# Kernel optimization log

Measured on AMD Instinct MI355X. Metric: run time of the kernel, lower is better.

The kernel has to match this reference:

```python
import jax, jax.numpy as jnp
import numpy as np
from math import sqrt

B, T, I, H, O, R = 128, 1000, 3, 512, 1, 2
NOISE_STD = 0.05
ALPHA = 0.2


def setup_inputs() -> dict:
    key = jax.random.key(0)
    ks = jax.random.split(key, 6)
    inp = jax.random.normal(ks[0], (B, T, I), dtype=jnp.float32)
    noise = jax.random.normal(ks[1], (B, T, H), dtype=jnp.float32)
    # parameters initialized as in the torch module
    wi = jax.random.normal(ks[2], (I, H), dtype=jnp.float32)
    si = jnp.ones((I,), dtype=jnp.float32)
    m = jax.random.normal(ks[3], (H, R), dtype=jnp.float32) * (1.0 / sqrt(H))
    n = jax.random.normal(ks[4], (H, R), dtype=jnp.float32) * (1.0 / sqrt(H))
    wo = jax.random.normal(ks[5], (H, O), dtype=jnp.float32) * (2.0 / H)
    so = jnp.ones((O,), dtype=jnp.float32)
    h0 = jnp.zeros((H,), dtype=jnp.float32)
    return {"input": inp, "noise": noise, "wi": wi, "si": si, "m": m,
            "n": n, "wo": wo, "so": so, "h0": h0}


def reference(input, noise, wi, si, m, n, wo, so, h0):
    # proxy parameters: wi_full = (wi.T * si).T, wo_full = wo * so
    wi_full = si[:, None] * wi          # (I, H)
    wo_full = wo * so                   # (H, O)
    batch = input.shape[0]
    h_init = jnp.broadcast_to(h0, (batch, h0.shape[0]))  # (B, H)

    def step(h, xs):
        x_t, z_t = xs                   # (B, I), (B, H)
        r = jnp.tanh(h)
        rec = (r @ n) @ m.T             # low-rank recurrence, (B, H)
        h_new = h + NOISE_STD * z_t + ALPHA * (-h + rec + x_t @ wi_full)
        out = jnp.tanh(h_new) @ wo_full  # (B, O)
        return h_new, (out, h_new)

    xs = (jnp.swapaxes(input, 0, 1), jnp.swapaxes(noise, 0, 1))  # time-major
    _, (outs, hs) = jax.lax.scan(step, h_init, xs)
    output = jnp.swapaxes(outs, 0, 1)               # (B, T, O)
    trajectories = jnp.concatenate(
        [h_init[:, None, :], jnp.swapaxes(hs, 0, 1)], axis=1)  # (B, T+1, H)
    return output, trajectories
```

## Files before the change

kernel.cpp:

```cpp
#include <hip/hip_runtime.h>
#include <stdint.h>

#define B_ 128
#define T_ 1000
#define H_ 512
#define PH 8
#define NPHASE 125

typedef float vfloat4 __attribute__((ext_vector_type(4)));

template <int CTRL>
__device__ __forceinline__ float dpp_add(float x) {
    int moved = __builtin_amdgcn_update_dpp(0, __float_as_int(x), CTRL, 0xf, 0xf, true);
    return x + __int_as_float(moved);
}

__device__ __forceinline__ void wave_reduce2(float& p0, float& p1) {
    p0 = dpp_add<0x111>(p0); p1 = dpp_add<0x111>(p1);
    p0 = dpp_add<0x112>(p0); p1 = dpp_add<0x112>(p1);
    p0 = dpp_add<0x114>(p0); p1 = dpp_add<0x114>(p1);
    p0 = dpp_add<0x118>(p0); p1 = dpp_add<0x118>(p1);
    p0 = dpp_add<0x142>(p0); p1 = dpp_add<0x142>(p1);
    p0 = dpp_add<0x143>(p0); p1 = dpp_add<0x143>(p1);
}

__device__ __forceinline__ float wave_reduce1(float p) {
    p = dpp_add<0x111>(p); p = dpp_add<0x112>(p); p = dpp_add<0x114>(p);
    p = dpp_add<0x118>(p); p = dpp_add<0x142>(p); p = dpp_add<0x143>(p);
    return p;
}

__device__ __forceinline__ float fast_tanh(float x) {
    float E = __builtin_amdgcn_exp2f(x * 2.885390081777927f);
    float r = __builtin_amdgcn_rcpf(E + 1.0f);
    return __builtin_fmaf(-2.0f, r, 1.0f);
}

__global__ __launch_bounds__(128, 1) void lowrank_rnn_kernel(
    const float* __restrict__ input,
    const float* __restrict__ noise,
    const float* __restrict__ wi,
    const float* __restrict__ si,
    const float* __restrict__ m,
    const float* __restrict__ n,
    const float* __restrict__ wo,
    const float* __restrict__ so,
    const float* __restrict__ h0,
    float* __restrict__ out)
{
    const int b    = blockIdx.x;
    const int tid  = threadIdx.x;
    const int wid  = tid >> 6;
    const int lane = tid & 63;
    const int j0   = lane * 8;

    __shared__ __align__(16) vfloat4 ub[2][PH][2][64];
    __shared__ __align__(16) vfloat4 rb[2][PH][2][64];
    __shared__ __align__(16) vfloat4 hb[2][PH][2][64];
    __shared__ __align__(16) vfloat4 rfin[2][64];
    __shared__ float os[T_ + 1];
    __shared__ int   flags[2];

    if (tid == 0) { flags[0] = 0; flags[1] = 0; }
    __syncthreads();
    volatile int* vprod = &flags[0];
    volatile int* vcons = &flags[1];

    if (wid == 1) {
        float wS0[8], wS1[8], wS2[8], wof[8];
        {
            const float so0 = so[0];
            #pragma unroll
            for (int i = 0; i < 3; ++i) {
                float s = 0.2f * si[i];
                float* dst = (i == 0) ? wS0 : (i == 1) ? wS1 : wS2;
                #pragma unroll
                for (int q = 0; q < 2; ++q) {
                    vfloat4 vw = *(const vfloat4*)(wi + i * H_ + j0 + 4 * q);
                    dst[4*q] = vw.x * s; dst[4*q+1] = vw.y * s;
                    dst[4*q+2] = vw.z * s; dst[4*q+3] = vw.w * s;
                }
            }
            #pragma unroll
            for (int q = 0; q < 2; ++q) {
                vfloat4 vw = *(const vfloat4*)(wo + j0 + 4 * q);
                wof[4*q] = vw.x * so0; wof[4*q+1] = vw.y * so0;
                wof[4*q+2] = vw.z * so0; wof[4*q+3] = vw.w * so0;
            }
        }
        const float* zb = noise + (size_t)b * T_ * H_ + j0;
        const float* xb = input + (size_t)b * T_ * 3;
        float* trajBase = out + (size_t)B_ * T_ + (size_t)b * (T_ + 1) * H_;

        {
            vfloat4 a = *(const vfloat4*)(h0 + j0);
            vfloat4 c = *(const vfloat4*)(h0 + j0 + 4);
            *(vfloat4*)(trajBase + j0)     = a;
            *(vfloat4*)(trajBase + j0 + 4) = c;
        }

        auto emit_phase = [&](int pp) {
            const int hf = pp & 1;
            #pragma unroll
            for (int s = 0; s < PH; ++s) {
                const int t = pp * PH + s;
                vfloat4 rl = rb[hf][s][0][lane];
                vfloat4 rh = rb[hf][s][1][lane];
                float p2 = rl.x * wof[0];
                p2 = __builtin_fmaf(rl.y, wof[1], p2);
                p2 = __builtin_fmaf(rl.z, wof[2], p2);
                p2 = __builtin_fmaf(rl.w, wof[3], p2);
                p2 = __builtin_fmaf(rh.x, wof[4], p2);
                p2 = __builtin_fmaf(rh.y, wof[5], p2);
                p2 = __builtin_fmaf(rh.z, wof[6], p2);
                p2 = __builtin_fmaf(rh.w, wof[7], p2);
                p2 = wave_reduce1(p2);
                if (lane == 63) os[t] = p2;
                vfloat4 hl = hb[hf][s][0][lane];
                vfloat4 hh = hb[hf][s][1][lane];
                float* tr = trajBase + (size_t)(t + 1) * H_ + j0;
                *(vfloat4*)tr       = hl;
                *(vfloat4*)(tr + 4) = hh;
            }
        };

        for (int q = 0; q < NPHASE; ++q) {
            if (q >= 2) {
                while (*vcons < q - 1) {}
                asm volatile("" ::: "memory");
            }
            vfloat4 zl[PH], zh[PH];
            #pragma unroll
            for (int s = 0; s < PH; ++s) {
                const float* g = zb + (size_t)(q * PH + s) * H_;
                zl[s] = *(const vfloat4*)g;
                zh[s] = *(const vfloat4*)(g + 4);
            }
            if (q >= 2) emit_phase(q - 2);
            const int half = q & 1;
            #pragma unroll
            for (int s = 0; s < PH; ++s) {
                const int t = q * PH + s;
                float x0 = xb[3*t], x1 = xb[3*t+1], x2 = xb[3*t+2];
                float zz[8] = {zl[s].x, zl[s].y, zl[s].z, zl[s].w,
                               zh[s].x, zh[s].y, zh[s].z, zh[s].w};
                float u[8];
                #pragma unroll
                for (int k = 0; k < 8; ++k) {
                    float xw = __builtin_fmaf(x0, wS0[k],
                               __builtin_fmaf(x1, wS1[k], x2 * wS2[k]));
                    u[k] = __builtin_fmaf(zz[k], 0.05f, xw);
                }
                vfloat4 ulo = {u[0], u[1], u[2], u[3]};
                vfloat4 uhi = {u[4], u[5], u[6], u[7]};
                ub[half][s][0][lane] = ulo;
                ub[half][s][1][lane] = uhi;
            }
            asm volatile("s_waitcnt lgkmcnt(0)" ::: "memory");
            if (lane == 0) *vprod = q + 1;
        }
        while (*vcons < NPHASE) {}
        asm volatile("" ::: "memory");
        emit_phase(NPHASE - 2);
        emit_phase(NPHASE - 1);
        while (*vcons < NPHASE + 1) {}
        asm volatile("" ::: "memory");
        {
            vfloat4 rl = rfin[0][lane], rh = rfin[1][lane];
            float p2 = rl.x * wof[0];
            p2 = __builtin_fmaf(rl.y, wof[1], p2);
            p2 = __builtin_fmaf(rl.z, wof[2], p2);
            p2 = __builtin_fmaf(rl.w, wof[3], p2);
            p2 = __builtin_fmaf(rh.x, wof[4], p2);
            p2 = __builtin_fmaf(rh.y, wof[5], p2);
            p2 = __builtin_fmaf(rh.z, wof[6], p2);
            p2 = __builtin_fmaf(rh.w, wof[7], p2);
            p2 = wave_reduce1(p2);
            if (lane == 63) os[T_] = p2;
        }
        asm volatile("s_waitcnt lgkmcnt(0)" ::: "memory");
        float* outp = out + (size_t)b * T_;
        for (int idx = lane; idx < T_; idx += 64)
            outp[idx] = os[idx + 1];
    } else {
        float h[8], n0[8], n1[8], m0S[8], m1S[8];
        {
            const float* nb = n + 2 * j0;
            const float* mb = m + 2 * j0;
            #pragma unroll
            for (int q = 0; q < 4; ++q) {
                vfloat4 vn = *(const vfloat4*)(nb + 4 * q);
                n0[2*q] = vn.x; n1[2*q] = vn.y; n0[2*q+1] = vn.z; n1[2*q+1] = vn.w;
                vfloat4 vm = *(const vfloat4*)(mb + 4 * q);
                m0S[2*q] = 0.2f * vm.x;   m1S[2*q] = 0.2f * vm.y;
                m0S[2*q+1] = 0.2f * vm.z; m1S[2*q+1] = 0.2f * vm.w;
            }
            #pragma unroll
            for (int q = 0; q < 2; ++q) {
                vfloat4 vh = *(const vfloat4*)(h0 + j0 + 4 * q);
                h[4*q] = vh.x; h[4*q+1] = vh.y; h[4*q+2] = vh.z; h[4*q+3] = vh.w;
            }
        }

        for (int p = 0; p < NPHASE; ++p) {
            while (*vprod < p + 1) {}
            asm volatile("" ::: "memory");
            const int half = p & 1;
            vfloat4 cul = ub[half][0][0][lane];
            vfloat4 cuh = ub[half][0][1][lane];
            #pragma unroll
            for (int s = 0; s < PH; ++s) {
                vfloat4 nul, nuh;
                if (s < PH - 1) {
                    nul = ub[half][s+1][0][lane];
                    nuh = ub[half][s+1][1][lane];
                }
                float r[8];
                #pragma unroll
                for (int k = 0; k < 8; ++k) r[k] = fast_tanh(h[k]);

                float p0 = r[0] * n0[0], p1 = r[0] * n1[0];
                #pragma unroll
                for (int k = 1; k < 8; ++k) {
                    p0 = __builtin_fmaf(r[k], n0[k], p0);
                    p1 = __builtin_fmaf(r[k], n1[k], p1);
                }
                wave_reduce2(p0, p1);

                float uu[8] = {cul.x, cul.y, cul.z, cul.w, cuh.x, cuh.y, cuh.z, cuh.w};
                float base[8];
                #pragma unroll
                for (int k = 0; k < 8; ++k)
                    base[k] = __builtin_fmaf(h[k], 0.8f, uu[k]);

                float a0 = __int_as_float(__builtin_amdgcn_readlane(__float_as_int(p0), 63));
                float a1 = __int_as_float(__builtin_amdgcn_readlane(__float_as_int(p1), 63));

                #pragma unroll
                for (int k = 0; k < 8; ++k)
                    h[k] = __builtin_fmaf(a0, m0S[k], __builtin_fmaf(a1, m1S[k], base[k]));

                vfloat4 rlo = {r[0], r[1], r[2], r[3]};
                vfloat4 rhi = {r[4], r[5], r[6], r[7]};
                rb[half][s][0][lane] = rlo;
                rb[half][s][1][lane] = rhi;
                vfloat4 hlo = {h[0], h[1], h[2], h[3]};
                vfloat4 hhi = {h[4], h[5], h[6], h[7]};
                hb[half][s][0][lane] = hlo;
                hb[half][s][1][lane] = hhi;

                cul = nul; cuh = nuh;
            }
            asm volatile("s_waitcnt lgkmcnt(0)" ::: "memory");
            if (lane == 0) *vcons = p + 1;
        }
        while (*vprod < NPHASE) {}
        asm volatile("" ::: "memory");
        float r[8];
        #pragma unroll
        for (int k = 0; k < 8; ++k) r[k] = fast_tanh(h[k]);
        vfloat4 rlo = {r[0], r[1], r[2], r[3]};
        vfloat4 rhi = {r[4], r[5], r[6], r[7]};
        rfin[0][lane] = rlo;
        rfin[1][lane] = rhi;
        asm volatile("s_waitcnt lgkmcnt(0)" ::: "memory");
        if (lane == 0) *vcons = NPHASE + 1;
    }
}

extern "C" void kernel_launch(void* const* d_in, const int* in_sizes, int n_in,
                              void* d_out, int out_size, void* d_ws, size_t ws_size,
                              hipStream_t stream) {
    const float* input = (const float*)d_in[0];
    const float* noise = (const float*)d_in[1];
    const float* wi    = (const float*)d_in[2];
    const float* si    = (const float*)d_in[3];
    const float* m     = (const float*)d_in[4];
    const float* n     = (const float*)d_in[5];
    const float* wo    = (const float*)d_in[6];
    const float* so    = (const float*)d_in[7];
    const float* h0    = (const float*)d_in[8];
    float* out = (float*)d_out;

    hipLaunchKernelGGL(lowrank_rnn_kernel, dim3(B_), dim3(128), 0, stream,
                       input, noise, wi, si, m, n, wo, so, h0, out);
}
```

Baseline: 295.8 us.

## Precompute tanh of base term off critical path and correct with polynomial

Splits h into base plus a low-rank correction and computes the exp/rcp for tanh(base) ahead of the wave reduction. tanh(h) at the next step is then recovered by a cheap Taylor expansion of exp on the small correction plus a Newton-style reciprocal refinement. The aim is to take the transcendental latency off the serial recurrence chain. The product sum is also rebalanced into a tree. This is an approximation whose accuracy depends on the correction staying small.

New measurement: 376.1 us. +27.1%, slower.

```diff
diff --git a/kernel.cpp b/kernel.cpp
--- a/kernel.cpp
+++ b/kernel.cpp
@@ -35,6 +35,9 @@
     float r = __builtin_amdgcn_rcpf(E + 1.0f);
     return __builtin_fmaf(-2.0f, r, 1.0f);
 }
+
+#define C2_ 2.885390081777927f
+#define C6_ 0.16666666666666666f
 
 __global__ __launch_bounds__(128, 1) void lowrank_rnn_kernel(
     const float* __restrict__ input,
@@ -183,14 +186,14 @@
         for (int idx = lane; idx < T_; idx += 64)
             outp[idx] = os[idx + 1];
     } else {
-        float h[8], n0[8], n1[8], m0S[8], m1S[8];
+        float h[8], n0v[8], n1v[8], m0S[8], m1S[8], R0[8], S0[8];
         {
             const float* nb = n + 2 * j0;
             const float* mb = m + 2 * j0;
             #pragma unroll
             for (int q = 0; q < 4; ++q) {
                 vfloat4 vn = *(const vfloat4*)(nb + 4 * q);
-                n0[2*q] = vn.x; n1[2*q] = vn.y; n0[2*q+1] = vn.z; n1[2*q+1] = vn.w;
+                n0v[2*q] = vn.x; n1v[2*q] = vn.y; n0v[2*q+1] = vn.z; n1v[2*q+1] = vn.w;
                 vfloat4 vm = *(const vfloat4*)(mb + 4 * q);
                 m0S[2*q] = 0.2f * vm.x;   m1S[2*q] = 0.2f * vm.y;
                 m0S[2*q+1] = 0.2f * vm.z; m1S[2*q+1] = 0.2f * vm.w;
@@ -200,7 +203,14 @@
                 vfloat4 vh = *(const vfloat4*)(h0 + j0 + 4 * q);
                 h[4*q] = vh.x; h[4*q+1] = vh.y; h[4*q+2] = vh.z; h[4*q+3] = vh.w;
             }
-        }
+            #pragma unroll
+            for (int k = 0; k < 8; ++k) {
+                float eb = __builtin_amdgcn_exp2f(h[k] * C2_);
+                float r0 = __builtin_amdgcn_rcpf(eb + 1.0f);
+                R0[k] = r0; S0[k] = 1.0f - r0;
+            }
+        }
+        float a0T = 0.0f, a1T = 0.0f;
 
         for (int p = 0; p < NPHASE; ++p) {
             while (*vprod < p + 1) {}
@@ -217,28 +227,46 @@
                 }
                 float r[8];
                 #pragma unroll
-                for (int k = 0; k < 8; ++k) r[k] = fast_tanh(h[k]);
-
-                float p0 = r[0] * n0[0], p1 = r[0] * n1[0];
-                #pragma unroll
-                for (int k = 1; k < 8; ++k) {
-                    p0 = __builtin_fmaf(r[k], n0[k], p0);
-                    p1 = __builtin_fmaf(r[k], n1[k], p1);
-                }
-                wave_reduce2(p0, p1);
+                for (int k = 0; k < 8; ++k) {
+                    float v  = __builtin_fmaf(a0T, m0S[k], a1T * m1S[k]);
+                    float t1 = __builtin_fmaf(v, C6_, 0.5f);
+                    float t2 = __builtin_fmaf(v, t1, 1.0f);
+                    float em = v * t2;
+                    float g  = S0[k] * em;
+                    float w1 = 1.0f - g;
+                    float w2 = __builtin_fmaf(-g, w1, 1.0f);
+                    float q  = __builtin_fmaf(-g, w2, 1.0f);
+                    float qq = q + q;
+                    r[k] = __builtin_fmaf(-R0[k], qq, 1.0f);
+                }
+                float u0[8], u1[8];
+                #pragma unroll
+                for (int k = 0; k < 8; ++k) { u0[k] = r[k] * n0v[k]; u1[k] = r[k] * n1v[k]; }
+                float p0 = ((u0[0]+u0[1]) + (u0[2]+u0[3])) + ((u0[4]+u0[5]) + (u0[6]+u0[7]));
+                float p1 = ((u1[0]+u1[1]) + (u1[2]+u1[3])) + ((u1[4]+u1[5]) + (u1[6]+u1[7]));
 
                 float uu[8] = {cul.x, cul.y, cul.z, cul.w, cuh.x, cuh.y, cuh.z, cuh.w};
-                float base[8];
+                float base[8], R0n[8], S0n[8];
                 #pragma unroll
                 for (int k = 0; k < 8; ++k)
                     base[k] = __builtin_fmaf(h[k], 0.8f, uu[k]);
-
+                #pragma unroll
+                for (int k = 0; k < 8; ++k) {
+                    float eb = __builtin_amdgcn_exp2f(base[k] * C2_);
+                    float r0 = __builtin_amdgcn_rcpf(eb + 1.0f);
+                    R0n[k] = r0; S0n[k] = 1.0f - r0;
+                }
+
+                wave_reduce2(p0, p1);
                 float a0 = __int_as_float(__builtin_amdgcn_readlane(__float_as_int(p0), 63));
                 float a1 = __int_as_float(__builtin_amdgcn_readlane(__float_as_int(p1), 63));
 
                 #pragma unroll
                 for (int k = 0; k < 8; ++k)
                     h[k] = __builtin_fmaf(a0, m0S[k], __builtin_fmaf(a1, m1S[k], base[k]));
+                a0T = a0 + a0; a1T = a1 + a1;
+                #pragma unroll
+                for (int k = 0; k < 8; ++k) { R0[k] = R0n[k]; S0[k] = S0n[k]; }
 
                 vfloat4 rlo = {r[0], r[1], r[2], r[3]};
                 vfloat4 rhi = {r[4], r[5], r[6], r[7]};
```

## Break serial recurrence dependency with Taylor-linearized lookahead of low-rank coefficients

Applied to the files above, without the earlier changes.

The compute wave no longer waits on a full tanh, dot and wave reduction before each step. It precomputes tanh of a predicted next state two steps ahead and keeps a first-order correction, using a Jacobian-like 2x2 matrix refreshed every four steps. That matrix gives the rank-2 coefficients from already-reduced quantities, taking the cross-lane reduction off the per-step critical path. State is also packed into float2 vectors to allow packed math, and the trajectory indexing is shifted with a separate final-state buffer. The linearization is an approximation of tanh, so it adds numerical error and many more VALU operations per step.

Result: slower. 357.1 us (+20.7%).

```diff
diff --git a/kernel.cpp b/kernel.cpp
--- a/kernel.cpp
+++ b/kernel.cpp
@@ -8,6 +8,7 @@
 #define NPHASE 125
 
 typedef float vfloat4 __attribute__((ext_vector_type(4)));
+typedef float vfloat2 __attribute__((ext_vector_type(2)));
 
 template <int CTRL>
 __device__ __forceinline__ float dpp_add(float x) {
@@ -24,6 +25,15 @@
     p0 = dpp_add<0x143>(p0); p1 = dpp_add<0x143>(p1);
 }
 
+__device__ __forceinline__ void wave_reduce4(float& a, float& b, float& c, float& d) {
+    a = dpp_add<0x111>(a); b = dpp_add<0x111>(b); c = dpp_add<0x111>(c); d = dpp_add<0x111>(d);
+    a = dpp_add<0x112>(a); b = dpp_add<0x112>(b); c = dpp_add<0x112>(c); d = dpp_add<0x112>(d);
+    a = dpp_add<0x114>(a); b = dpp_add<0x114>(b); c = dpp_add<0x114>(c); d = dpp_add<0x114>(d);
+    a = dpp_add<0x118>(a); b = dpp_add<0x118>(b); c = dpp_add<0x118>(c); d = dpp_add<0x118>(d);
+    a = dpp_add<0x142>(a); b = dpp_add<0x142>(b); c = dpp_add<0x142>(c); d = dpp_add<0x142>(d);
+    a = dpp_add<0x143>(a); b = dpp_add<0x143>(b); c = dpp_add<0x143>(c); d = dpp_add<0x143>(d);
+}
+
 __device__ __forceinline__ float wave_reduce1(float p) {
     p = dpp_add<0x111>(p); p = dpp_add<0x112>(p); p = dpp_add<0x114>(p);
     p = dpp_add<0x118>(p); p = dpp_add<0x142>(p); p = dpp_add<0x143>(p);
@@ -36,17 +46,24 @@
     return __builtin_fmaf(-2.0f, r, 1.0f);
 }
 
+#define C2_ 2.885390081777927f
+#define RL63(x) __int_as_float(__builtin_amdgcn_readlane(__float_as_int(x), 63))
+
+__device__ __forceinline__ vfloat2 bc2(float x) { vfloat2 v = {x, x}; return v; }
+__device__ __forceinline__ vfloat2 th2(vfloat2 b) {
+    vfloat2 x2 = b * C2_;
+    vfloat2 E  = {__builtin_amdgcn_exp2f(x2.x), __builtin_amdgcn_exp2f(x2.y)};
+    vfloat2 D  = E + 1.0f;
+    vfloat2 R  = {__builtin_amdgcn_rcpf(D.x), __builtin_amdgcn_rcpf(D.y)};
+    return bc2(-2.0f) * R + 1.0f;
+}
+
 __global__ __launch_bounds__(128, 1) void lowrank_rnn_kernel(
-    const float* __restrict__ input,
-    const float* __restrict__ noise,
-    const float* __restrict__ wi,
-    const float* __restrict__ si,
-    const float* __restrict__ m,
-    const float* __restrict__ n,
-    const float* __restrict__ wo,
-    const float* __restrict__ so,
-    const float* __restrict__ h0,
-    float* __restrict__ out)
+    const float* __restrict__ input, const float* __restrict__ noise,
+    const float* __restrict__ wi, const float* __restrict__ si,
+    const float* __restrict__ m, const float* __restrict__ n,
+    const float* __restrict__ wo, const float* __restrict__ so,
+    const float* __restrict__ h0, float* __restrict__ out)
 {
     const int b    = blockIdx.x;
     const int tid  = threadIdx.x;
@@ -58,6 +75,7 @@
     __shared__ __align__(16) vfloat4 rb[2][PH][2][64];
     __shared__ __align__(16) vfloat4 hb[2][PH][2][64];
     __shared__ __align__(16) vfloat4 rfin[2][64];
+    __shared__ __align__(16) vfloat4 hfin[2][64];
     __shared__ float os[T_ + 1];
     __shared__ int   flags[2];
 
@@ -118,7 +136,7 @@
                 if (lane == 63) os[t] = p2;
                 vfloat4 hl = hb[hf][s][0][lane];
                 vfloat4 hh = hb[hf][s][1][lane];
-                float* tr = trajBase + (size_t)(t + 1) * H_ + j0;
+                float* tr = trajBase + (size_t)t * H_ + j0;
                 *(vfloat4*)tr       = hl;
                 *(vfloat4*)(tr + 4) = hh;
             }
@@ -177,94 +195,228 @@
             p2 = __builtin_fmaf(rh.w, wof[7], p2);
             p2 = wave_reduce1(p2);
             if (lane == 63) os[T_] = p2;
+            float* tr = trajBase + (size_t)T_ * H_ + j0;
+            *(vfloat4*)tr       = hfin[0][lane];
+            *(vfloat4*)(tr + 4) = hfin[1][lane];
         }
         asm volatile("s_waitcnt lgkmcnt(0)" ::: "memory");
         float* outp = out + (size_t)b * T_;
         for (int idx = lane; idx < T_; idx += 64)
             outp[idx] = os[idx + 1];
     } else {
-        float h[8], n0[8], n1[8], m0S[8], m1S[8];
+        vfloat2 m0S[4], m1S[4], n0v[4], n1v[4];
+        vfloat2 basep[4], Tk0[4], Tk1[4], Dk0[4], Dk1[4], ucur[4];
+        float cA0=0, cA1=0, cB0=0, cB1=0, qa0=0, qa1=0, qa2=0, qa3=0;
+        float A00, A01, A10, A11;
+        float a1_0, a1_1, a2_0, a2_1, C0cur, C1cur;
+        vfloat2 h0v[4];
         {
             const float* nb = n + 2 * j0;
             const float* mb = m + 2 * j0;
             #pragma unroll
             for (int q = 0; q < 4; ++q) {
                 vfloat4 vn = *(const vfloat4*)(nb + 4 * q);
-                n0[2*q] = vn.x; n1[2*q] = vn.y; n0[2*q+1] = vn.z; n1[2*q+1] = vn.w;
+                vfloat2 a = {vn.x, vn.z}; n0v[q] = a;
+                vfloat2 c = {vn.y, vn.w}; n1v[q] = c;
                 vfloat4 vm = *(const vfloat4*)(mb + 4 * q);
-                m0S[2*q] = 0.2f * vm.x;   m1S[2*q] = 0.2f * vm.y;
-                m0S[2*q+1] = 0.2f * vm.z; m1S[2*q+1] = 0.2f * vm.w;
+                vfloat2 d = {0.2f * vm.x, 0.2f * vm.z}; m0S[q] = d;
+                vfloat2 e = {0.2f * vm.y, 0.2f * vm.w}; m1S[q] = e;
             }
             #pragma unroll
             for (int q = 0; q < 2; ++q) {
                 vfloat4 vh = *(const vfloat4*)(h0 + j0 + 4 * q);
-                h[4*q] = vh.x; h[4*q+1] = vh.y; h[4*q+2] = vh.z; h[4*q+3] = vh.w;
-            }
-        }
-
-        for (int p = 0; p < NPHASE; ++p) {
+                vfloat2 lo = {vh.x, vh.y}, hi = {vh.z, vh.w};
+                h0v[2*q] = lo; h0v[2*q+1] = hi;
+            }
+        }
+        #define HORIZ(dst, A_, B_) { \
+            vfloat2 q01_ = A_[1]*B_[1] + A_[0]*B_[0]; \
+            vfloat2 q23_ = A_[3]*B_[3] + A_[2]*B_[2]; \
+            vfloat2 qq_ = q01_ + q23_; dst = qq_.x + qq_.y; }
+        #define SHIP(ring, hf, sl, V_) { \
+            vfloat4 lo_ = {V_[0].x, V_[0].y, V_[1].x, V_[1].y}; \
+            vfloat4 hi_ = {V_[2].x, V_[2].y, V_[3].x, V_[3].y}; \
+            ring[hf][sl][0][lane] = lo_; ring[hf][sl][1][lane] = hi_; }
+        #define RDU(dst, hf, sl) { \
+            vfloat4 lo_ = ub[hf][sl][0][lane]; vfloat4 hi_ = ub[hf][sl][1][lane]; \
+            vfloat2 t0_ = {lo_.x, lo_.y}; dst[0] = t0_; \
+            vfloat2 t1_ = {lo_.z, lo_.w}; dst[1] = t1_; \
+            vfloat2 t2_ = {hi_.x, hi_.y}; dst[2] = t2_; \
+            vfloat2 t3_ = {hi_.z, hi_.w}; dst[3] = t3_; }
+
+        while (*vprod < 1) {}
+        asm volatile("" ::: "memory");
+        vfloat2 u0v[4], u1v[4], u2v[4];
+        RDU(u0v, 0, 0); RDU(u1v, 0, 1); RDU(u2v, 0, 2);
+        float a0_0, a0_1;
+        {
+            vfloat2 r0v[4], T0v[4], D0v[4], base0c[4];
+            #pragma unroll
+            for (int j = 0; j < 4; ++j) r0v[j] = th2(h0v[j]);
+            SHIP(rb, 0, 0, r0v); SHIP(hb, 0, 0, h0v);
+            float p0, p1; HORIZ(p0, r0v, n0v); HORIZ(p1, r0v, n1v);
+            wave_reduce2(p0, p1);
+            a0_0 = RL63(p0); a0_1 = RL63(p1);
+            #pragma unroll
+            for (int j = 0; j < 4; ++j) { base0c[j] = h0v[j] * 0.8f + u0v[j]; basep[j] = base0c[j]; }
+            #pragma unroll
+            for (int j = 0; j < 4; ++j) { T0v[j] = th2(base0c[j]); D0v[j] = 1.0f - T0v[j]*T0v[j]; }
+            float c10, c11; HORIZ(c10, T0v, n0v); HORIZ(c11, T0v, n1v);
+            vfloat2 e0[4], e1[4];
+            #pragma unroll
+            for (int j = 0; j < 4; ++j) { e0[j] = D0v[j]*m0S[j]; e1[j] = D0v[j]*m1S[j]; }
+            float q0, q1, q2, q3;
+            HORIZ(q0, e0, n0v); HORIZ(q1, e1, n0v); HORIZ(q2, e0, n1v); HORIZ(q3, e1, n1v);
+            wave_reduce2(c10, c11); wave_reduce4(q0, q1, q2, q3);
+            float C1_0 = RL63(c10), C1_1 = RL63(c11);
+            A00 = RL63(q0); A01 = RL63(q1); A10 = RL63(q2); A11 = RL63(q3);
+            #pragma unroll
+            for (int j = 0; j < 4; ++j) {
+                vfloat2 be = base0c[j] * 0.8f + u1v[j];
+                vfloat2 T = th2(be); Tk0[j] = T; Dk0[j] = 1.0f - T*T;
+            }
+            HORIZ(cA0, Tk0, n0v); HORIZ(cA1, Tk0, n1v);
+            wave_reduce2(cA0, cA1);
+            float w0 = a0_0, w1 = a0_1;
+            float at0 = C1_0 + A00*w0 + A01*w1;
+            float at1 = C1_1 + A10*w0 + A11*w1;
+            vfloat2 ab0 = bc2(a0_0), ab1 = bc2(a0_1);
+            vfloat2 h1v[4], r1v[4];
+            #pragma unroll
+            for (int j = 0; j < 4; ++j) {
+                vfloat2 dl = ab0*m0S[j] + ab1*m1S[j];
+                h1v[j] = basep[j] + dl;
+                vfloat2 t1 = T0v[j]*dl;
+                vfloat2 ee = dl - t1*dl;
+                r1v[j] = D0v[j]*ee + T0v[j];
+            }
+            SHIP(hb, 0, 1, h1v); SHIP(rb, 0, 1, r1v);
+            #pragma unroll
+            for (int j = 0; j < 4; ++j) basep[j] = h1v[j]*0.8f + u1v[j];
+            #pragma unroll
+            for (int j = 0; j < 4; ++j) {
+                vfloat2 be = basep[j]*0.8f + u2v[j];
+                vfloat2 T = th2(be); Tk1[j] = T; Dk1[j] = 1.0f - T*T;
+            }
+            HORIZ(cB0, Tk1, n0v); HORIZ(cB1, Tk1, n1v);
+            wave_reduce2(cB0, cB1);
+            C0cur = RL63(cA0); C1cur = RL63(cA1);
+            a2_0 = a0_0; a2_1 = a0_1; a1_0 = at0; a1_1 = at1;
+            #pragma unroll
+            for (int j = 0; j < 4; ++j) ucur[j] = u2v[j];
+        }
+
+        #define CSTEP(S_, HF_, UH_, US_, SPIN_, RLA_) { \
+            if (SPIN_) { while (*vprod < (SPIN_)) {} asm volatile("" ::: "memory"); } \
+            vfloat2 unv[4]; RDU(unv, (UH_), (US_)); \
+            float Cn0, Cn1; \
+            if (((S_) & 1) == 0) { Cn0 = RL63(cB0); Cn1 = RL63(cB1); } \
+            else                 { Cn0 = RL63(cA0); Cn1 = RL63(cA1); } \
+            if (((S_) % 4) == 2 && (RLA_)) { \
+                A00 = RL63(qa0); A01 = RL63(qa1); A10 = RL63(qa2); A11 = RL63(qa3); } \
+            float w0 = __builtin_fmaf(0.8f, a2_0, a1_0); \
+            float w1 = __builtin_fmaf(0.8f, a2_1, a1_1); \
+            float at0 = __builtin_fmaf(A00, w0, __builtin_fmaf(A01, w1, C0cur)); \
+            float at1 = __builtin_fmaf(A10, w0, __builtin_fmaf(A11, w1, C1cur)); \
+            vfloat2 ab0 = bc2(a1_0), ab1 = bc2(a1_1); \
+            vfloat2 wb0 = bc2(w0),  wb1 = bc2(w1); \
+            vfloat2 hv[4], rv[4], Tn[4], Dn[4]; \
+            _Pragma("unroll") \
+            for (int j = 0; j < 4; ++j) { \
+                vfloat2 dl = ab0*m0S[j] + ab1*m1S[j]; \
+                hv[j] = basep[j] + dl; \
+                vfloat2 ep = wb0*m0S[j] + wb1*m1S[j]; \
+                vfloat2 Tp = ((S_) & 1) ? Tk1[j] : Tk0[j]; \
+                vfloat2 Dp = ((S_) & 1) ? Dk1[j] : Dk0[j]; \
+                vfloat2 t1 = Tp*ep; \
+                vfloat2 ee = ep - t1*ep; \
+                rv[j] = Dp*ee + Tp; \
+            } \
+            SHIP(hb, (HF_), (S_), hv); SHIP(rb, (HF_), (S_), rv); \
+            _Pragma("unroll") \
+            for (int j = 0; j < 4; ++j) { \
+                basep[j] = hv[j]*0.8f + ucur[j]; \
+                vfloat2 be = basep[j]*0.8f + unv[j]; \
+                vfloat2 T = th2(be); \
+                Tn[j] = T; Dn[j] = 1.0f - T*T; \
+                if ((S_) & 1) { Tk1[j] = T; Dk1[j] = Dn[j]; } \
+                else          { Tk0[j] = T; Dk0[j] = Dn[j]; } \
+                ucur[j] = unv[j]; \
+            } \
+            float pc0, pc1; HORIZ(pc0, Tn, n0v); HORIZ(pc1, Tn, n1v); \
+            if (((S_) & 1) == 0) { cA0 = pc0; cA1 = pc1; wave_reduce2(cA0, cA1); } \
+            else                 { cB0 = pc0; cB1 = pc1; wave_reduce2(cB0, cB1); } \
+            if (((S_) % 4) == 0) { \
+                vfloat2 e0[4], e1[4]; \
+                _Pragma("unroll") \
+                for (int j = 0; j < 4; ++j) { e0[j] = Dn[j]*m0S[j]; e1[j] = Dn[j]*m1S[j]; } \
+                HORIZ(qa0, e0, n0v); HORIZ(qa1, e1, n0v); \
+                HORIZ(qa2, e0, n1v); HORIZ(qa3, e1, n1v); \
+                wave_reduce4(qa0, qa1, qa2, qa3); \
+            } \
+            a2_0 = a1_0; a2_1 = a1_1; a1_0 = at0; a1_1 = at1; \
+            C0cur = Cn0; C1cur = Cn1; }
+
+        CSTEP(2, 0, 0, 3, 0, 0)
+        CSTEP(3, 0, 0, 4, 0, 1)
+        CSTEP(4, 0, 0, 5, 0, 1)
+        CSTEP(5, 0, 0, 6, 0, 1)
+        CSTEP(6, 0, 0, 7, 0, 1)
+        CSTEP(7, 0, 1, 0, 2, 1)
+        asm volatile("s_waitcnt lgkmcnt(0)" ::: "memory");
+        if (lane == 0) *vcons = 1;
+
+        for (int p = 1; p < NPHASE - 1; ++p) {
             while (*vprod < p + 1) {}
             asm volatile("" ::: "memory");
             const int half = p & 1;
-            vfloat4 cul = ub[half][0][0][lane];
-            vfloat4 cuh = ub[half][0][1][lane];
-            #pragma unroll
-            for (int s = 0; s < PH; ++s) {
-                vfloat4 nul, nuh;
-                if (s < PH - 1) {
-                    nul = ub[half][s+1][0][lane];
-                    nuh = ub[half][s+1][1][lane];
-                }
-                float r[8];
-                #pragma unroll
-                for (int k = 0; k < 8; ++k) r[k] = fast_tanh(h[k]);
-
-                float p0 = r[0] * n0[0], p1 = r[0] * n1[0];
-                #pragma unroll
-                for (int k = 1; k < 8; ++k) {
-                    p0 = __builtin_fmaf(r[k], n0[k], p0);
-                    p1 = __builtin_fmaf(r[k], n1[k], p1);
-                }
-                wave_reduce2(p0, p1);
-
-                float uu[8] = {cul.x, cul.y, cul.z, cul.w, cuh.x, cuh.y, cuh.z, cuh.w};
-                float base[8];
-                #pragma unroll
-                for (int k = 0; k < 8; ++k)
-                    base[k] = __builtin_fmaf(h[k], 0.8f, uu[k]);
-
-                float a0 = __int_as_float(__builtin_amdgcn_readlane(__float_as_int(p0), 63));
-                float a1 = __int_as_float(__builtin_amdgcn_readlane(__float_as_int(p1), 63));
-
-                #pragma unroll
-                for (int k = 0; k < 8; ++k)
-                    h[k] = __builtin_fmaf(a0, m0S[k], __builtin_fmaf(a1, m1S[k], base[k]));
-
-                vfloat4 rlo = {r[0], r[1], r[2], r[3]};
-                vfloat4 rhi = {r[4], r[5], r[6], r[7]};
-                rb[half][s][0][lane] = rlo;
-                rb[half][s][1][lane] = rhi;
-                vfloat4 hlo = {h[0], h[1], h[2], h[3]};
-                vfloat4 hhi = {h[4], h[5], h[6], h[7]};
-                hb[half][s][0][lane] = hlo;
-                hb[half][s][1][lane] = hhi;
-
-                cul = nul; cuh = nuh;
-            }
+            CSTEP(0, half, half, 1, 0, 1)
+            CSTEP(1, half, half, 2, 0, 1)
+            CSTEP(2, half, half, 3, 0, 1)
+            CSTEP(3, half, half, 4, 0, 1)
+            CSTEP(4, half, half, 5, 0, 1)
+            CSTEP(5, half, half, 6, 0, 1)
+            CSTEP(6, half, half, 7, 0, 1)
+            CSTEP(7, half, half ^ 1, 0, p + 2, 1)
             asm volatile("s_waitcnt lgkmcnt(0)" ::: "memory");
             if (lane == 0) *vcons = p + 1;
         }
-        while (*vprod < NPHASE) {}
-        asm volatile("" ::: "memory");
-        float r[8];
-        #pragma unroll
-        for (int k = 0; k < 8; ++k) r[k] = fast_tanh(h[k]);
-        vfloat4 rlo = {r[0], r[1], r[2], r[3]};
-        vfloat4 rhi = {r[4], r[5], r[6], r[7]};
-        rfin[0][lane] = rlo;
-        rfin[1][lane] = rhi;
-        asm volatile("s_waitcnt lgkmcnt(0)" ::: "memory");
-        if (lane == 0) *vcons = NPHASE + 1;
+        {
+            while (*vprod < NPHASE) {}
+            asm volatile("" ::: "memory");
+            CSTEP(0, 0, 0, 1, 0, 1)
+            CSTEP(1, 0, 0, 2, 0, 1)
+            CSTEP(2, 0, 0, 3, 0, 1)
+            CSTEP(3, 0, 0, 4, 0, 1)
+            CSTEP(4, 0, 0, 5, 0, 1)
+            CSTEP(5, 0, 0, 6, 0, 1)
+            CSTEP(6, 0, 0, 7, 0, 1)
+            CSTEP(7, 0, 0, 7, 0, 1)
+            asm volatile("s_waitcnt lgkmcnt(0)" ::: "memory");
+            if (lane == 0) *vcons = NPHASE;
+        }
+        {
+            vfloat2 ab0 = bc2(a1_0), ab1 = bc2(a1_1);
+            vfloat2 hT[4], rT[4];
+            #pragma unroll
+            for (int j = 0; j < 4; ++j) {
+                vfloat2 dl = ab0*m0S[j] + ab1*m1S[j];
+                hT[j] = basep[j] + dl;
+                rT[j] = th2(hT[j]);
+            }
+            vfloat4 rlo = {rT[0].x, rT[0].y, rT[1].x, rT[1].y};
+            vfloat4 rhi = {rT[2].x, rT[2].y, rT[3].x, rT[3].y};
+            rfin[0][lane] = rlo; rfin[1][lane] = rhi;
+            vfloat4 hlo = {hT[0].x, hT[0].y, hT[1].x, hT[1].y};
+            vfloat4 hhi = {hT[2].x, hT[2].y, hT[3].x, hT[3].y};
+            hfin[0][lane] = hlo; hfin[1][lane] = hhi;
+            asm volatile("s_waitcnt lgkmcnt(0)" ::: "memory");
+            if (lane == 0) *vcons = NPHASE + 1;
+        }
+        #undef CSTEP
+        #undef HORIZ
+        #undef SHIP
+        #undef RDU
     }
 }
 
```
